# Kernel tuning notes

Measured on AMD Instinct MI355X. Metric: run time of the kernel, lower is better.

Reference implementation:

```python
import jax, jax.numpy as jnp
import numpy as np

B, N, CIN = 16, 2048, 6
R, G = 20, 128          # Reeb nodes, scc group size
F1 = 1000
NCLASS = 40


def pairwise_distance(pc):
    # pc: (B, N, C) -> adjacency exp(-squared_euclidean_dist), (B, N, N)
    inner = -2.0 * jnp.matmul(pc, pc.transpose(0, 2, 1))
    sq = jnp.sum(pc * pc, axis=-1, keepdims=True)
    return jnp.exp(-(sq + inner + sq.transpose(0, 2, 1)))


def get_laplacian(adj):
    # normalized Laplacian L = I - D^{-1/2} A D^{-1/2}
    d_inv = 1.0 / jnp.sqrt(jnp.sum(adj, axis=-1))
    eye = jnp.eye(adj.shape[-1], dtype=adj.dtype)
    return eye - d_inv[:, :, None] * adj * d_inv[:, None, :]


def cheb_conv(x, L, K, W, b):
    # Chebyshev recurrence: T0=x, T1=Lx, Tk=2L T_{k-1} - T_{k-2}
    xs = [x]
    if K > 1:
        x0, x1 = x, jnp.matmul(L, x)
        xs.append(x1)
        for _ in range(2, K):
            x2 = 2.0 * jnp.matmul(L, x1) - x0
            xs.append(x2)
            x0, x1 = x1, x2
    Bb, Nn, Fin = x.shape
    # torch stacks on dim0 then permutes to (B,N,Fin,K) before reshape -> K is minor axis
    xk = jnp.stack(xs, axis=-1).reshape(Bb, Nn, Fin * K)
    return jnp.matmul(xk, W) + b


def setup_inputs() -> dict:
    key = jax.random.key(0)
    ks = jax.random.split(key, 10)

    def glorot(k, shape):
        lim = np.sqrt(6.0 / (shape[0] + shape[1])).astype(np.float32)
        return jax.random.uniform(k, shape, jnp.float32, -lim, lim)

    return {
        "x": jax.random.normal(ks[0], (B, N, CIN), jnp.float32),
        "laplacian_Reeb": jax.random.normal(ks[1], (B, R, R), jnp.float32),
        "sccs": jax.random.randint(ks[2], (B, R, G), 0, N),
        "W1": glorot(ks[3], (CIN * 3, F1)), "b1": jnp.zeros((F1,), jnp.float32),
        "W2": glorot(ks[4], (F1 * 3, F1)), "b2": jnp.zeros((F1,), jnp.float32),
        "Wr": glorot(ks[5], (F1 * 6, F1)), "br": jnp.zeros((F1,), jnp.float32),
        "Wfc1": glorot(ks[6], (2 * F1, 512)), "bfc1": jnp.zeros((512,), jnp.float32),
        "Wfc2": glorot(ks[7], (512, 128)), "bfc2": jnp.zeros((128,), jnp.float32),
        "Wfc3": glorot(ks[8], (128, NCLASS)), "bfc3": jnp.zeros((NCLASS,), jnp.float32),
        "k": 30, "batch_size": B, "num_points": N,
    }


def reference(x, laplacian_Reeb, sccs, W1, b1, W2, b2, Wr, br,
              Wfc1, bfc1, Wfc2, bfc2, Wfc3, bfc3, k, batch_size, num_points):
    regs = []
    # graph Laplacian from point features (torch.no_grad)
    L = jax.lax.stop_gradient(get_laplacian(pairwise_distance(x)))
    out = jax.nn.relu(cheb_conv(x, L, 3, W1, b1))
    regs.append(jnp.linalg.norm(jnp.matmul(jnp.matmul(out.transpose(0, 2, 1), L), x)))

    # Reeb pooling: per Reeb node, max over its scc vertex group (torch.no_grad)
    v = out[jnp.arange(out.shape[0])[:, None, None], sccs]  # (B, R, G, F1)
    vertices_Reeb = jax.lax.stop_gradient(jnp.max(v, axis=2))  # (B, R, F1)

    # second dynamic-graph Laplacian on features (torch.no_grad)
    L2 = jax.lax.stop_gradient(get_laplacian(pairwise_distance(out)))
    out2 = jax.nn.relu(cheb_conv(out, L2, 3, W2, b2))
    regs.append(jnp.linalg.norm(jnp.matmul(jnp.matmul(out2.transpose(0, 2, 1), L2), x)))

    out_Reeb = jax.nn.relu(cheb_conv(vertices_Reeb, laplacian_Reeb, 6, Wr, br))

    g = jnp.max(out2, axis=1)           # (B, F1) global max pool
    g_Reeb = jnp.max(out_Reeb, axis=1)  # (B, F1)
    feat = jnp.concatenate([g_Reeb, g], axis=1)  # (B, 2000)

    h = jax.nn.relu(jnp.matmul(feat, Wfc1) + bfc1)
    regs += [jnp.sum(Wfc1[:, 0] ** 2), bfc1[0] ** 2]  # norm(weight.data[0])**2
    h = jax.nn.relu(jnp.matmul(h, Wfc2) + bfc2)
    regs += [jnp.sum(Wfc2[:, 0] ** 2), bfc2[0] ** 2]
    out_final = jnp.matmul(h, Wfc3) + bfc3
    regs += [jnp.sum(Wfc3[:, 0] ** 2), bfc3[0] ** 2]

    return out_final, jnp.stack(regs)
```

## Files before the change

kernel.cpp:

```cpp
#include <hip/hip_runtime.h>
#include <stdint.h>

#define DI __device__ __forceinline__

typedef __bf16 bf16x8 __attribute__((ext_vector_type(8)));
typedef float f32x4 __attribute__((ext_vector_type(4)));
typedef unsigned short u16x4 __attribute__((ext_vector_type(4)));
typedef unsigned short u16x8 __attribute__((ext_vector_type(8)));

static constexpr int BB = 16;
static constexpr int NP = 2048;
static constexpr int FP = 1024;
static constexpr int K3 = 3072;
static constexpr int RR = 20;
static constexpr int GG = 128;
static constexpr int RK = 6144;
static constexpr int MRp = 384;
static constexpr int NJ = 32;
static constexpr int NI = 8;
static constexpr int NJ2 = 8;

DI float b2f(unsigned short u) {
    unsigned v = ((unsigned)u) << 16;
    return __builtin_bit_cast(float, v);
}
DI unsigned short f2b(float f) {
    unsigned u = __builtin_bit_cast(unsigned, f);
    unsigned r = (u + 0x7FFFu + ((u >> 16) & 1u)) >> 16;
    return (unsigned short)r;
}

DI void glds16(const unsigned short* g, unsigned short* l) {
    __builtin_amdgcn_global_load_lds(
        (const __attribute__((address_space(1))) void*)g,
        (__attribute__((address_space(3))) void*)l, 16, 0, 0);
}

#define SYNC_VM4() asm volatile("s_waitcnt vmcnt(4)\n\ts_barrier" ::: "memory")
#define SYNC_VM0() asm volatile("s_waitcnt vmcnt(0)\n\ts_barrier" ::: "memory")
#define SYNC_LGKM() asm volatile("s_waitcnt lgkmcnt(0)\n\ts_barrier" ::: "memory")

enum { EADJ = 0, ELAP1 = 1, ELAP2 = 2, EBRELU = 3 };

template <int EPI>
__global__ __launch_bounds__(256) void gemm_bt(
    const unsigned short* __restrict__ A, long sA, int lda,
    const unsigned short* __restrict__ Bt, long sB, int ldb,
    unsigned short* __restrict__ C, long sC, int ldc, int K,
    const float* __restrict__ sq,
    float* __restrict__ rowsum,
    const unsigned short* __restrict__ aux, long sAux, int ldaux,
    const float* __restrict__ bias, int biasN)
{
    __shared__ unsigned short smem[16384];
    const int tid = threadIdx.x;

    int gx = gridDim.x, gy = gridDim.y;
    int flat = blockIdx.x + gx * (blockIdx.y + gy * blockIdx.z);
    int tpb = gx * gy;
    int T = tpb * gridDim.z;
    int bz, ty, tx;
    if (((T & 7) == 0) && ((gx & 7) == 0)) {
        int per = T >> 3;
        int g = (flat & 7) * per + (flat >> 3);
        bz = g / tpb;
        int t = g - bz * tpb;
        int strip = gy << 3;
        int cg = t / strip;
        int r = t - cg * strip;
        ty = r >> 3;
        tx = (cg << 3) + (r & 7);
    } else {
        bz = blockIdx.z; ty = blockIdx.y; tx = blockIdx.x;
    }
    const int rowBase = ty * 128;
    const int colBase = tx * 128;
    const unsigned short* Ab = A + (long)bz * sA + (long)rowBase * lda;
    const unsigned short* Bb = Bt + (long)bz * sB + (long)colBase * ldb;

    const int lane = tid & 63;
    const int q = lane >> 4;
    const int l15 = lane & 15;
    const int wave = tid >> 6;
    const int wr = (wave >> 1) * 64;
    const int wc = (wave & 1) * 64;

    const int r0 = tid & 127, c0 = tid >> 7;
    const int c1 = c0 + 2;

    f32x4 acc[4][4];
#pragma unroll
    for (int i = 0; i < 4; i++)
#pragma unroll
        for (int j = 0; j < 4; j++) acc[i][j] = f32x4{0.f, 0.f, 0.f, 0.f};

    const int nIter = K >> 5;
    glds16(Ab + (long)r0 * lda + c0 * 8, smem + tid * 8);
    glds16(Ab + (long)r0 * lda + c1 * 8, smem + (tid + 256) * 8);
    glds16(Bb + (long)r0 * ldb + c0 * 8, smem + 4096 + tid * 8);
    glds16(Bb + (long)r0 * ldb + c1 * 8, smem + 4096 + (tid + 256) * 8);

    for (int it = 0; it < nIter; ++it) {
        unsigned short* cur = smem + ((it & 1) << 13);
        unsigned short* nxt = smem + (((it + 1) & 1) << 13);
        if (it + 1 < nIter) {
            const int kb = (it + 1) << 5;
            glds16(Ab + (long)r0 * lda + kb + c0 * 8, nxt + tid * 8);
            glds16(Ab + (long)r0 * lda + kb + c1 * 8, nxt + (tid + 256) * 8);
            glds16(Bb + (long)r0 * ldb + kb + c0 * 8, nxt + 4096 + tid * 8);
            glds16(Bb + (long)r0 * ldb + kb + c1 * 8, nxt + 4096 + (tid + 256) * 8);
            SYNC_VM4();
        } else {
            SYNC_VM0();
        }
        bf16x8 af[4], bfr[4];
#pragma unroll
        for (int mi = 0; mi < 4; mi++)
            af[mi] = *(const bf16x8*)(cur + (q * 128 + wr + mi * 16 + l15) * 8);
#pragma unroll
        for (int ni = 0; ni < 4; ni++)
            bfr[ni] = *(const bf16x8*)(cur + 4096 + (q * 128 + wc + ni * 16 + l15) * 8);
#pragma unroll
        for (int mi = 0; mi < 4; mi++)
#pragma unroll
            for (int ni = 0; ni < 4; ni++)
                acc[mi][ni] = __builtin_amdgcn_mfma_f32_16x16x32_bf16(
                    af[mi], bfr[ni], acc[mi][ni], 0, 0, 0);
        SYNC_LGKM();
    }

    const float* sqb = (EPI != EBRELU) ? (sq + (long)bz * NP) : nullptr;
#pragma unroll
    for (int mi = 0; mi < 4; mi++) {
#pragma unroll
        for (int rg = 0; rg < 4; rg++) {
            const int grow = rowBase + wr + mi * 16 + q * 4 + rg;
            float rsumv = 0.f;
            float di = 0.f;
            if (EPI == ELAP1 || EPI == ELAP2) di = sqb[grow];
#pragma unroll
            for (int ni = 0; ni < 4; ni++) {
                const int gcol = colBase + wc + ni * 16 + l15;
                float v = acc[mi][ni][rg];
                long cidx = (long)bz * sC + (long)grow * ldc + gcol;
                if (EPI == EADJ) {
                    float e = __expf(2.f * v - sqb[grow] - sqb[gcol]);
                    C[cidx] = f2b(e);
                    rsumv += e;
                } else if (EPI == ELAP1) {
                    float o = b2f(aux[(long)bz * sAux + (long)grow * ldaux + gcol]);
                    C[cidx] = f2b(o - di * v);
                } else if (EPI == ELAP2) {
                    long abase = (long)bz * sAux + (long)grow * ldaux + gcol;
                    float o0 = b2f(aux[abase]);
                    float o1 = b2f(aux[abase + 1024]);
                    C[cidx] = f2b(2.f * (o1 - di * v) - o0);
                } else {
                    float bv = (gcol < biasN) ? bias[gcol] : 0.f;
                    float o = v + bv;
                    C[cidx] = f2b(o > 0.f ? o : 0.f);
                }
            }
            if (EPI == EADJ) {
                rsumv += __shfl_xor(rsumv, 1);
                rsumv += __shfl_xor(rsumv, 2);
                rsumv += __shfl_xor(rsumv, 4);
                rsumv += __shfl_xor(rsumv, 8);
                if (l15 == 0) atomicAdd(&rowsum[(long)bz * NP + grow], rsumv);
            }
        }
    }
}

__global__ __launch_bounds__(256) void k_trs(
    const unsigned short* __restrict__ src, long sS, int ldS,
    const float* __restrict__ dv,
    unsigned short* __restrict__ dst, long sD, int ldD)
{
    __shared__ unsigned short t[64][72];
    const int b = blockIdx.z;
    const int c0 = blockIdx.x * 64, r0 = blockIdx.y * 64;
    const unsigned short* S = src + (long)b * sS;
    const float* dvb = dv + (long)b * NP;
    unsigned short* D = dst + (long)b * sD;
    const int tx = threadIdx.x & 7, ty = threadIdx.x >> 3;
#pragma unroll
    for (int p = 0; p < 2; p++) {
        int r = ty + p * 32;
        float s = dvb[r0 + r];
        u16x8 v = *(const u16x8*)(S + (long)(r0 + r) * ldS + c0 + tx * 8);
#pragma unroll
        for (int k = 0; k < 8; k++) t[tx * 8 + k][r] = f2b(s * b2f(v[k]));
    }
    __syncthreads();
#pragma unroll
    for (int p = 0; p < 2; p++) {
        int r = ty + p * 32;
        u16x8 v;
#pragma unroll
        for (int k = 0; k < 8; k++) v[k] = t[r][tx * 8 + k];
        *(u16x8*)(D + (long)(c0 + r) * ldD + r0 + tx * 8) = v;
    }
}

__global__ void k_trf32(const float* __restrict__ src, int R, int C,
                        float* __restrict__ dst)
{
    __shared__ float t[32][33];
    const int c0 = blockIdx.x * 32, r0 = blockIdx.y * 32;
#pragma unroll
    for (int p = 0; p < 4; p++) {
        int r = r0 + threadIdx.y + p * 8;
        int c = c0 + threadIdx.x;
        t[threadIdx.y + p * 8][threadIdx.x] =
            (r < R && c < C) ? src[(long)r * C + c] : 0.f;
    }
    __syncthreads();
#pragma unroll
    for (int p = 0; p < 4; p++) {
        int c = c0 + threadIdx.y + p * 8;
        int r = r0 + threadIdx.x;
        if (c < C && r < R) dst[(long)c * R + r] = t[threadIdx.x][threadIdx.y + p * 8];
    }
}

__global__ __launch_bounds__(256) void k_wperm(
    const float* __restrict__ W, unsigned short* __restrict__ dst, int KK, int dstld)
{
    __shared__ float tile[64][65];
    const int o0 = blockIdx.x * 64;
    const int kk0 = blockIdx.y * 64;
    const int s = kk0 >> 10;
    const int fbase = kk0 & 1023;
    const int ci = threadIdx.x & 63;
    const int ri = threadIdx.x >> 6;
#pragma unroll 4
    for (int p = 0; p < 16; p++) {
        int fi = fbase + ri + p * 4;
        int oi = o0 + ci;
        float v = 0.f;
        if (fi < 1000 && oi < 1000) v = W[((long)fi * KK + s) * 1000 + oi];
        tile[ri + p * 4][ci] = v;
    }
    __syncthreads();
#pragma unroll 4
    for (int p = 0; p < 16; p++) {
        int orow = ri + p * 4;
        dst[(long)(o0 + orow) * dstld + kk0 + ci] = f2b(tile[ci][orow]);
    }
}

__global__ void k_zinit(float* __restrict__ rs2, float* __restrict__ g,
                        float* __restrict__ racc, unsigned short* __restrict__ catrpad,
                        float* __restrict__ dv1, float* __restrict__ xacc1,
                        float* __restrict__ xacc2, float* __restrict__ yacc1,
                        float* __restrict__ yacc2, float* __restrict__ l2acc,
                        float* __restrict__ vr)
{
    long i = (long)blockIdx.x * 256 + threadIdx.x;
    if (i < (long)BB * NP) { rs2[i] = 0.f; dv1[i] = 0.f; }
    if (i < (long)BB * FP) g[i] = 0.f;
    if (i < 64) racc[i] = 0.f;
    if (i < (long)(MRp - 320) * RK) catrpad[i] = 0;
    if (i < (long)BB * 6 * NP) { xacc1[i] = 0.f; xacc2[i] = 0.f; l2acc[i] = 0.f; }
    if (i < (long)BB * 6 * FP) { yacc1[i] = 0.f; yacc2[i] = 0.f; }
    if (i < (long)BB * RR * FP) vr[i] = 0.f;
}

__global__ void k_xprep(const float* __restrict__ x, float* __restrict__ x6t,
                        float* __restrict__ sqx)
{
    const int b = blockIdx.y;
    const int j = blockIdx.x * 256 + threadIdx.x;
    float s = 0.f;
#pragma unroll
    for (int c = 0; c < 6; c++) {
        float v = x[((long)b * NP + j) * 6 + c];
        x6t[(long)b * 6 * NP + c * NP + j] = v;
        s += v * v;
    }
    sqx[(long)b * NP + j] = s;
}

template <int MODE>
__global__ __launch_bounds__(256) void k_lapj(
    const float* __restrict__ x6t, const float* __restrict__ sqx,
    const float* __restrict__ dv1, const float* __restrict__ srct,
    float* __restrict__ acc)
{
    const int b = blockIdx.z;
    const int row = blockIdx.x * 256 + threadIdx.x;
    const int j0 = blockIdx.y * (NP / NJ);
    const float* xt = x6t + (long)b * 6 * NP;
    const float* sq = sqx + (long)b * NP;
    float xi[6];
#pragma unroll
    for (int c = 0; c < 6; c++) xi[c] = xt[c * NP + row];
    const float sqi = sq[row];
    const float* dv = (MODE >= 1) ? (dv1 + (long)b * NP) : nullptr;
    const float* st = (MODE >= 1) ? (srct + (long)b * 6 * NP) : nullptr;
    float s0 = 0.f;
    float sc[6] = {0, 0, 0, 0, 0, 0};
    for (int j = j0; j < j0 + NP / NJ; j++) {
        float dot = 0.f;
#pragma unroll
        for (int c = 0; c < 6; c++) dot += xi[c] * xt[c * NP + j];
        float e = __expf(2.f * dot - sqi - sq[j]);
        if (MODE == 0) {
            s0 += e;
        } else {
            float wgt = e * dv[j];
#pragma unroll
            for (int c = 0; c < 6; c++) sc[c] += wgt * st[c * NP + j];
        }
    }
    if (MODE == 0) {
        atomicAdd(&acc[(long)b * NP + row], s0);
    } else {
#pragma unroll
        for (int c = 0; c < 6; c++)
            atomicAdd(&acc[(long)b * 6 * NP + c * NP + row], sc[c]);
    }
}

template <int MODE>
__global__ void k_lfin(const float* __restrict__ x6t, const float* __restrict__ dv1,
                       const float* __restrict__ xacc, const float* __restrict__ x1t6,
                       float* __restrict__ outv)
{
    const int b = blockIdx.y;
    const int row = blockIdx.x * 256 + threadIdx.x;
    const float di = dv1[(long)b * NP + row];
#pragma unroll
    for (int c = 0; c < 6; c++) {
        long idx = (long)b * 6 * NP + c * NP + row;
        float xi = x6t[idx];
        float sc = xacc[idx];
        if (MODE == 1) outv[idx] = xi - di * sc;
        else           outv[idx] = 2.f * (x1t6[idx] - di * sc) - xi;
    }
}

__global__ __launch_bounds__(256) void k_adjx(
    const unsigned short* __restrict__ adj, const float* __restrict__ dv,
    const float* __restrict__ x6t, float* __restrict__ l2acc)
{
    __shared__ float xs[6][256];
    __shared__ float dvs[256];
    __shared__ float lsum[64][4][6];
    const int b = blockIdx.z;
    const int j0 = blockIdx.y * (NP / NJ2);
    if (threadIdx.x < 256) dvs[threadIdx.x] = dv[(long)b * NP + j0 + threadIdx.x];
    for (int e = threadIdx.x; e < 6 * 256; e += 256) {
        int c = e >> 8, j = e & 255;
        xs[c][j] = x6t[(long)b * 6 * NP + c * NP + j0 + j];
    }
    __syncthreads();
    const int ty = threadIdx.x >> 2;
    const int tx = threadIdx.x & 3;
    const int grow = blockIdx.x * 64 + ty;
    const unsigned short* rowp = adj + (long)b * NP * NP + (long)grow * NP + j0;
    float sc[6] = {0, 0, 0, 0, 0, 0};
    for (int it = 0; it < 8; it++) {
        int col = it * 32 + tx * 8;
        u16x8 a8 = *(const u16x8*)(rowp + col);
#pragma unroll
        for (int k = 0; k < 8; k++) {
            float w = b2f(a8[k]) * dvs[col + k];
#pragma unroll
            for (int c = 0; c < 6; c++) sc[c] += w * xs[c][col + k];
        }
    }
#pragma unroll
    for (int c = 0; c < 6; c++) lsum[ty][tx][c] = sc[c];
    __syncthreads();
    for (int e = threadIdx.x; e < 64 * 6; e += 256) {
        int row = e / 6, c = e % 6;
        float t = lsum[row][0][c] + lsum[row][1][c] + lsum[row][2][c] + lsum[row][3][c];
        atomicAdd(&l2acc[(long)b * 6 * NP + (long)c * NP + blockIdx.x * 64 + row], t);
    }
}

__global__ __launch_bounds__(256) void k_cheb1(
    const float* __restrict__ x, const float* __restrict__ x1t6,
    const float* __restrict__ x2t6, const float* __restrict__ W1,
    const float* __restrict__ b1, unsigned short* __restrict__ cat)
{
    __shared__ float xk[128 * 18];
    const int b = blockIdx.z;
    const int n0 = blockIdx.x * 128;
    const int f0 = blockIdx.y * 256;
    for (int e = threadIdx.x; e < 128 * 18; e += 256) {
        int rown = e / 18, c18 = e % 18;
        int cc = c18 / 3, kk = c18 % 3;
        int n = n0 + rown;
        float v;
        if (kk == 0) v = x[((long)b * NP + n) * 6 + cc];
        else if (kk == 1) v = x1t6[(long)b * 6 * NP + cc * NP + n];
        else v = x2t6[(long)b * 6 * NP + cc * NP + n];
        xk[e] = v;
    }
    __syncthreads();
    for (int gi = threadIdx.x; gi < 128 * 64; gi += 256) {
        int rown = gi >> 6;
        int f4 = f0 + (gi & 63) * 4;
        float a0 = 0, a1 = 0, a2 = 0, a3 = 0;
        if (f4 < 1000) {
            a0 = b1[f4]; a1 = b1[f4 + 1]; a2 = b1[f4 + 2]; a3 = b1[f4 + 3];
#pragma unroll
            for (int cI = 0; cI < 18; cI++) {
                float xv = xk[rown * 18 + cI];
                f32x4 w = *(const f32x4*)(W1 + cI * 1000 + f4);
                a0 += xv * w[0]; a1 += xv * w[1]; a2 += xv * w[2]; a3 += xv * w[3];
            }
            a0 = a0 > 0 ? a0 : 0; a1 = a1 > 0 ? a1 : 0;
            a2 = a2 > 0 ? a2 : 0; a3 = a3 > 0 ? a3 : 0;
        }
        u16x4 o;
        o[0] = f2b(a0); o[1] = f2b(a1); o[2] = f2b(a2); o[3] = f2b(a3);
        *(u16x4*)(cat + (long)b * NP * K3 + (long)(n0 + rown) * K3 + f4) = o;
    }
}

__global__ void k_sqc(const unsigned short* __restrict__ cat, float* __restrict__ sqc)
{
    __shared__ float red[256];
    const int b = blockIdx.y;
    const int rloc = threadIdx.x >> 4;
    const int r = blockIdx.x * 16 + rloc;
    const int tx = threadIdx.x & 15;
    const unsigned short* p = cat + (long)b * NP * K3 + (long)r * K3;
    float s = 0.f;
    for (int it = 0; it < 8; it++) {
        int cc = it * 128 + tx * 8;
        u16x8 v = *(const u16x8*)(p + cc);
#pragma unroll
        for (int k = 0; k < 8; k++) { float f = b2f(v[k]); s += f * f; }
    }
    red[threadIdx.x] = s;
    __syncthreads();
    if (tx == 0) {
        float t = 0.f;
#pragma unroll
        for (int k = 0; k < 16; k++) t += red[rloc * 16 + k];
        sqc[(long)b * NP + r] = t;
    }
}

__global__ void k_rsqrt(float* __restrict__ p) {
    int i = blockIdx.x * 256 + threadIdx.x;
    p[i] = rsqrtf(p[i]);
}

__global__ void k_vr(const unsigned short* __restrict__ cat,
                     const int* __restrict__ sccs, float* __restrict__ vr)
{
    const int b = blockIdx.y, r = blockIdx.x;
    const int g0 = blockIdx.z * (GG / 4);
    const int f4 = threadIdx.x * 4;
    const int* sp = sccs + ((long)b * RR + r) * GG;
    float m0 = 0.f, m1 = 0.f, m2 = 0.f, m3 = 0.f;
    for (int g = g0; g < g0 + GG / 4; g++) {
        int idx = sp[g];
        u16x4 v = *(const u16x4*)(cat + ((long)b * NP + idx) * K3 + f4);
        m0 = fmaxf(m0, b2f(v[0])); m1 = fmaxf(m1, b2f(v[1]));
        m2 = fmaxf(m2, b2f(v[2])); m3 = fmaxf(m3, b2f(v[3]));
    }
    float* op = vr + ((long)b * RR + r) * FP + f4;
    atomicMax((int*)&op[0], __float_as_int(m0));
    atomicMax((int*)&op[1], __float_as_int(m1));
    atomicMax((int*)&op[2], __float_as_int(m2));
    atomicMax((int*)&op[3], __float_as_int(m3));
}

__global__ __launch_bounds__(256) void k_reeb(
    const float* __restrict__ vr, const float* __restrict__ lapR,
    unsigned short* __restrict__ catr)
{
    __shared__ float Lr[RR * RR];
    const int b = blockIdx.y;
    for (int e = threadIdx.x; e < RR * RR; e += 256) Lr[e] = lapR[(long)b * RR * RR + e];
    __syncthreads();
    const int f = blockIdx.x * 256 + threadIdx.x;
    float xa[RR], xb[RR], xc[RR];
#pragma unroll
    for (int r = 0; r < RR; r++) xa[r] = vr[((long)b * RR + r) * FP + f];
#pragma unroll
    for (int r = 0; r < RR; r++) catr[((long)b * RR + r) * RK + f] = f2b(xa[r]);
#pragma unroll
    for (int r = 0; r < RR; r++) {
        float s = 0.f;
#pragma unroll
        for (int qq = 0; qq < RR; qq++) s += Lr[r * RR + qq] * xa[qq];
        xb[r] = s;
    }
#pragma unroll
    for (int r = 0; r < RR; r++) catr[((long)b * RR + r) * RK + FP + f] = f2b(xb[r]);
    for (int st = 2; st < 6; st++) {
#pragma unroll
        for (int r = 0; r < RR; r++) {
            float s = 0.f;
#pragma unroll
            for (int qq = 0; qq < RR; qq++) s += Lr[r * RR + qq] * xb[qq];
            xc[r] = 2.f * s - xa[r];
        }
#pragma unroll
        for (int r = 0; r < RR; r++)
            catr[((long)b * RR + r) * RK + st * FP + f] = f2b(xc[r]);
#pragma unroll
        for (int r = 0; r < RR; r++) { xa[r] = xb[r]; xb[r] = xc[r]; }
    }
}

__global__ void k_gmax(const unsigned short* __restrict__ out2, float* __restrict__ g)
{
    const int b = blockIdx.z;
    const int f = blockIdx.x * 256 + threadIdx.x;
    const int n0 = blockIdx.y * 256;
    float m = 0.f;
    for (int n = n0; n < n0 + 256; n++)
        m = fmaxf(m, b2f(out2[((long)b * NP + n) * FP + f]));
    if (f < 1000) atomicMax((int*)&g[(long)b * FP + f], __float_as_int(m));
}

__global__ void k_grmax(const unsigned short* __restrict__ outr, float* __restrict__ gr)
{
    const int b = blockIdx.y;
    const int f = blockIdx.x * 256 + threadIdx.x;
    float m = -1e30f;
    for (int r = 0; r < RR; r++)
        m = fmaxf(m, b2f(outr[((long)b * RR + r) * FP + f]));
    gr[(long)b * FP + f] = (f < 1000) ? m : 0.f;
}

__global__ __launch_bounds__(256) void k_rnacc(
    const unsigned short* __restrict__ mat, long sM, int ldm,
    const float* __restrict__ vt6, float* __restrict__ yacc)
{
    const int b = blockIdx.z;
    const int f = blockIdx.x * 256 + threadIdx.x;
    const int i0 = blockIdx.y * (NP / NI);
    const unsigned short* mp = mat + (long)b * sM + f;
    const float* vp = vt6 + (long)b * 6 * NP;
    float a[6] = {0, 0, 0, 0, 0, 0};
    for (int i = i0; i < i0 + NP / NI; i++) {
        float o = b2f(mp[(long)i * ldm]);
#pragma unroll
        for (int c = 0; c < 6; c++) a[c] += o * vp[c * NP + i];
    }
#pragma unroll
    for (int c = 0; c < 6; c++)
        atomicAdd(&yacc[((long)b * 6 + c) * FP + f], a[c]);
}

__global__ void k_rnred(const float* __restrict__ yacc1,
                        const float* __restrict__ yacc2, float* __restrict__ racc)
{
    __shared__ float red[256];
    const float* y = (blockIdx.x == 0) ? yacc1 : yacc2;
    const long tot = (long)BB * 6 * FP;
    const long per = tot / 16;
    const long e0 = blockIdx.y * per;
    float s = 0.f;
    for (long e = e0 + threadIdx.x; e < e0 + per; e += 256) {
        float v = y[e];
        s += v * v;
    }
    red[threadIdx.x] = s;
    __syncthreads();
    for (int st = 128; st > 0; st >>= 1) {
        if (threadIdx.x < st) red[threadIdx.x] += red[threadIdx.x + st];
        __syncthreads();
    }
    if (threadIdx.x == 0) atomicAdd(&racc[blockIdx.x], red[0]);
}

__global__ __launch_bounds__(256) void k_fc1w(
    const float* __restrict__ gr, const float* __restrict__ g,
    const float* __restrict__ WT1, const float* __restrict__ bias,
    float* __restrict__ h1)
{
    const int b = blockIdx.y;
    const int lane = threadIdx.x & 63;
    const int o = blockIdx.x * 4 + (threadIdx.x >> 6);
    const float* wt = WT1 + (long)o * 2000;
    const float* grp = gr + (long)b * FP;
    const float* gp = g + (long)b * FP;
    float s = 0.f;
    for (int j0 = 0; j0 < 2000; j0 += 64) {
        int j = j0 + lane;
        if (j < 2000) {
            float fv = (j < 1000) ? grp[j] : gp[j - 1000];
            s += fv * wt[j];
        }
    }
#pragma unroll
    for (int d = 1; d < 64; d <<= 1) s += __shfl_xor(s, d);
    if (lane == 0) {
        float v = s + bias[o];
        h1[(long)b * 512 + o] = v > 0.f ? v : 0.f;
    }
}

__global__ __launch_bounds__(256) void k_fc2w(
    const float* __restrict__ h1, const float* __restrict__ WT2,
    const float* __restrict__ bias, float* __restrict__ h2)
{
    const int b = blockIdx.y;
    const int lane = threadIdx.x & 63;
    const int o = blockIdx.x * 4 + (threadIdx.x >> 6);
    const float* wt = WT2 + (long)o * 512;
    const float* hp = h1 + (long)b * 512;
    float s = 0.f;
#pragma unroll
    for (int j0 = 0; j0 < 512; j0 += 64) s += hp[j0 + lane] * wt[j0 + lane];
#pragma unroll
    for (int d = 1; d < 64; d <<= 1) s += __shfl_xor(s, d);
    if (lane == 0) {
        float v = s + bias[o];
        h2[(long)b * 128 + o] = v > 0.f ? v : 0.f;
    }
}

__global__ void k_tail(const float* __restrict__ h2, const float* __restrict__ Wfc3,
                       const float* __restrict__ bfc3, const float* __restrict__ Wfc1,
                       const float* __restrict__ bfc1, const float* __restrict__ Wfc2,
                       const float* __restrict__ bfc2, const float* __restrict__ racc,
                       float* __restrict__ out)
{
    if (blockIdx.x == 0) {
        for (int e = threadIdx.x; e < 640; e += 256) {
            int row = e / 40, o = e % 40;
            float s = bfc3[o];
            for (int j = 0; j < 128; j++) s += h2[row * 128 + j] * Wfc3[j * 40 + o];
            out[e] = s;
        }
        return;
    }
    __shared__ float red[256];
    float s = 0.f;
    if (blockIdx.x == 1) {
        for (int j = threadIdx.x; j < 2000; j += 256) { float w = Wfc1[j * 512]; s += w * w; }
    } else if (blockIdx.x == 2) {
        for (int j = threadIdx.x; j < 512; j += 256) { float w = Wfc2[j * 128]; s += w * w; }
    } else {
        for (int j = threadIdx.x; j < 128; j += 256) { float w = Wfc3[j * 40]; s += w * w; }
    }
    red[threadIdx.x] = s;
    __syncthreads();
    for (int st = 128; st > 0; st >>= 1) {
        if (threadIdx.x < st) red[threadIdx.x] += red[threadIdx.x + st];
        __syncthreads();
    }
    if (threadIdx.x == 0) {
        if (blockIdx.x == 1) out[642] = red[0];
        else if (blockIdx.x == 2) out[644] = red[0];
        else {
            out[646] = red[0];
            out[640] = sqrtf(racc[0]);
            out[641] = sqrtf(racc[1]);
            out[643] = bfc1[0] * bfc1[0];
            out[645] = bfc2[0] * bfc2[0];
            out[647] = bfc3[0] * bfc3[0];
        }
    }
}

extern "C" void kernel_launch(void* const* d_in, const int* in_sizes, int n_in,
                              void* d_out, int out_size, void* d_ws, size_t ws_size,
                              hipStream_t stream)
{
    (void)in_sizes; (void)n_in; (void)out_size;
    const float* x    = (const float*)d_in[0];
    const float* lapR = (const float*)d_in[1];
    const int*   sccs = (const int*)d_in[2];
    const float* W1   = (const float*)d_in[3];
    const float* b1   = (const float*)d_in[4];
    const float* W2   = (const float*)d_in[5];
    const float* b2   = (const float*)d_in[6];
    const float* Wr   = (const float*)d_in[7];
    const float* br   = (const float*)d_in[8];
    const float* Wfc1 = (const float*)d_in[9];
    const float* bfc1 = (const float*)d_in[10];
    const float* Wfc2 = (const float*)d_in[11];
    const float* bfc2 = (const float*)d_in[12];
    const float* Wfc3 = (const float*)d_in[13];
    const float* bfc3 = (const float*)d_in[14];
    float* out = (float*)d_out;

    char* w = (char*)d_ws;
    size_t used = 0;
    auto alloc = [&](size_t bytes) {
        char* p = w + used;
        used += (bytes + 255) & ~(size_t)255;
        return p;
    };
    unsigned short* w2pt = (unsigned short*)alloc((size_t)FP * K3 * 2);
    unsigned short* wrpt = (unsigned short*)alloc((size_t)FP * RK * 2);
    unsigned short* catr = (unsigned short*)alloc((size_t)MRp * RK * 2);
    unsigned short* outr = (unsigned short*)alloc((size_t)MRp * FP * 2);
    float* vr   = (float*)alloc((size_t)BB * RR * FP * 4);
    float* x6t  = (float*)alloc((size_t)BB * 6 * NP * 4);
    float* sqx  = (float*)alloc((size_t)BB * NP * 4);
    float* dv1  = (float*)alloc((size_t)BB * NP * 4);
    float* x1t6 = (float*)alloc((size_t)BB * 6 * NP * 4);
    float* x2t6 = (float*)alloc((size_t)BB * 6 * NP * 4);
    float* xacc1= (float*)alloc((size_t)BB * 6 * NP * 4);
    float* xacc2= (float*)alloc((size_t)BB * 6 * NP * 4);
    float* l2acc= (float*)alloc((size_t)BB * 6 * NP * 4);
    float* sqc  = (float*)alloc((size_t)BB * NP * 4);
    float* rs2  = (float*)alloc((size_t)BB * NP * 4);
    float* l2xt6= (float*)alloc((size_t)BB * 6 * NP * 4);
    float* g    = (float*)alloc((size_t)BB * FP * 4);
    float* gr   = (float*)alloc((size_t)BB * FP * 4);
    float* h1   = (float*)alloc((size_t)BB * 512 * 4);
    float* h2   = (float*)alloc((size_t)BB * 128 * 4);
    float* racc = (float*)alloc(256);
    float* WT1  = (float*)alloc((size_t)512 * 2000 * 4);
    float* WT2  = (float*)alloc((size_t)128 * 512 * 4);
    float* yacc1= (float*)alloc((size_t)BB * 6 * FP * 4);
    float* yacc2= (float*)alloc((size_t)BB * 6 * FP * 4);

    const size_t PCAT = (size_t)NP * K3 * 2;
    const size_t PA   = (size_t)NP * NP * 2;
    const size_t PTT  = (size_t)FP * NP * 2;
    int C = 16;
    while (C > 1 && used + (size_t)C * (PCAT + PA + PTT) + 4096 > ws_size) C >>= 1;
    if (used + (size_t)C * (PCAT + PA + PTT) + 4096 > ws_size) return;

    unsigned short* cat_c = (unsigned short*)alloc((size_t)C * PCAT);
    unsigned short* a_c   = (unsigned short*)alloc((size_t)C * PA);
    unsigned short* tt_c  = (unsigned short*)alloc((size_t)C * PTT);
    unsigned short* out2_c = a_c;

    const long sCat = (long)NP * K3;
    const long sL2  = (long)NP * NP;
    const long sTT  = (long)FP * NP;
    const long sO2  = (long)NP * FP;

    k_zinit<<<dim3(1536), 256, 0, stream>>>(rs2, g, racc, catr + (size_t)320 * RK,
                                            dv1, xacc1, xacc2, yacc1, yacc2, l2acc, vr);

    k_wperm<<<dim3(16, K3 / 64), 256, 0, stream>>>(W2, w2pt, 3, K3);
    k_wperm<<<dim3(16, RK / 64), 256, 0, stream>>>(Wr, wrpt, 6, RK);
    k_trf32<<<dim3(16, 63), dim3(32, 8), 0, stream>>>(Wfc1, 2000, 512, WT1);
    k_trf32<<<dim3(4, 16), dim3(32, 8), 0, stream>>>(Wfc2, 512, 128, WT2);

    k_xprep<<<dim3(8, BB), 256, 0, stream>>>(x, x6t, sqx);
    k_lapj<0><<<dim3(8, NJ, BB), 256, 0, stream>>>(x6t, sqx, nullptr, nullptr, dv1);
    k_rsqrt<<<dim3(BB * NP / 256), 256, 0, stream>>>(dv1);
    k_lapj<1><<<dim3(8, NJ, BB), 256, 0, stream>>>(x6t, sqx, dv1, x6t, xacc1);
    k_lfin<1><<<dim3(8, BB), 256, 0, stream>>>(x6t, dv1, xacc1, nullptr, x1t6);
    k_lapj<2><<<dim3(8, NJ, BB), 256, 0, stream>>>(x6t, sqx, dv1, x1t6, xacc2);
    k_lfin<2><<<dim3(8, BB), 256, 0, stream>>>(x6t, dv1, xacc2, x1t6, x2t6);

    for (int c0 = 0; c0 < BB; c0 += C) {
        const float* xc  = x     + (long)c0 * NP * 6;
        const float* x6c = x6t   + (long)c0 * 6 * NP;
        const float* x1c = x1t6  + (long)c0 * 6 * NP;
        const float* x2c = x2t6  + (long)c0 * 6 * NP;
        float*       sqcc= sqc   + (long)c0 * NP;
        float*       rsc = rs2   + (long)c0 * NP;
        float*       l2ac= l2acc + (long)c0 * 6 * NP;
        float*       l2xc= l2xt6 + (long)c0 * 6 * NP;

        k_cheb1<<<dim3(16, 4, C), 256, 0, stream>>>(xc, x1c, x2c, W1, b1, cat_c);
        k_sqc<<<dim3(NP / 16, C), 256, 0, stream>>>(cat_c, sqcc);

        gemm_bt<EADJ><<<dim3(16, 16, C), 256, 0, stream>>>(
            cat_c, sCat, K3, cat_c, sCat, K3, a_c, sL2, NP, FP,
            sqcc, rsc, nullptr, 0, 0, nullptr, 0);
        k_rsqrt<<<dim3(C * NP / 256), 256, 0, stream>>>(rsc);

        k_adjx<<<dim3(NP / 64, NJ2, C), 256, 0, stream>>>(a_c, rsc, x6c, l2ac);
        k_lfin<1><<<dim3(8, C), 256, 0, stream>>>(x6c, rsc, l2ac, nullptr, l2xc);

        k_trs<<<dim3(16, 32, C), 256, 0, stream>>>(cat_c, sCat, K3, rsc, tt_c, sTT, NP);
        gemm_bt<ELAP1><<<dim3(8, 16, C), 256, 0, stream>>>(
            a_c, sL2, NP, tt_c, sTT, NP, cat_c + 1024, sCat, K3, NP,
            rsc, nullptr, cat_c, sCat, K3, nullptr, 0);

        k_trs<<<dim3(16, 32, C), 256, 0, stream>>>(cat_c + 1024, sCat, K3, rsc, tt_c, sTT, NP);
        gemm_bt<ELAP2><<<dim3(8, 16, C), 256, 0, stream>>>(
            a_c, sL2, NP, tt_c, sTT, NP, cat_c + 2048, sCat, K3, NP,
            rsc, nullptr, cat_c, sCat, K3, nullptr, 0);

        gemm_bt<EBRELU><<<dim3(8, 16, C), 256, 0, stream>>>(
            cat_c, sCat, K3, w2pt, 0, K3, out2_c, sO2, FP, K3,
            nullptr, nullptr, nullptr, 0, 0, b2, 1000);

        k_vr<<<dim3(RR, C, 4), 256, 0, stream>>>(
            cat_c, sccs + (long)c0 * RR * GG, vr + (long)c0 * RR * FP);
        k_gmax<<<dim3(4, 8, C), 256, 0, stream>>>(out2_c, g + (long)c0 * FP);
        k_rnacc<<<dim3(4, NI, C), 256, 0, stream>>>(
            cat_c, sCat, K3, x1c, yacc1 + (long)c0 * 6 * FP);
        k_rnacc<<<dim3(4, NI, C), 256, 0, stream>>>(
            out2_c, sO2, FP, l2xc, yacc2 + (long)c0 * 6 * FP);
    }

    k_reeb<<<dim3(4, BB), 256, 0, stream>>>(vr, lapR, catr);
    gemm_bt<EBRELU><<<dim3(8, 3, 1), 256, 0, stream>>>(
        catr, 0, RK, wrpt, 0, RK, outr, 0, FP, RK,
        nullptr, nullptr, nullptr, 0, 0, br, 1000);
    k_grmax<<<dim3(4, BB), 256, 0, stream>>>(outr, gr);

    k_rnred<<<dim3(2, 16), 256, 0, stream>>>(yacc1, yacc2, racc);
    k_fc1w<<<dim3(128, BB), 256, 0, stream>>>(gr, g, WT1, bfc1, h1);
    k_fc2w<<<dim3(32, BB), 256, 0, stream>>>(h1, WT2, bfc2, h2);
    k_tail<<<dim3(4), 256, 0, stream>>>(h2, Wfc3, bfc3, Wfc1, bfc1, Wfc2, bfc2, racc, out);
}
```

Before: 2.235 ms.

## Exploit adjacency symmetry, fuse row norms and global max, split-K Reeb GEMM

The adjacency GEMM now computes only the upper-triangular 128x128 tiles (136 of 256). Each off-diagonal tile is also written transposed through padded shared memory, and its column sums are added into the row sums. The squared-norm kernel is folded into the Chebyshev layer-1 kernel, and the global max over out2 is folded into the regularizer accumulation kernel. The small Reeb GEMM is split four ways along K with fp32 atomics, followed by a bias/ReLU finish kernel. These changes remove redundant GEMM work and extra passes over memory, at the cost of atomics, a larger shared buffer and a serial tile-index decode.

```diff
diff --git a/kernel.cpp b/kernel.cpp
--- a/kernel.cpp
+++ b/kernel.cpp
@@ -19,6 +19,7 @@
 static constexpr int NJ = 32;
 static constexpr int NI = 8;
 static constexpr int NJ2 = 8;
+static constexpr int TPAD = 132;
 
 DI float b2f(unsigned short u) {
     unsigned v = ((unsigned)u) << 16;
@@ -40,7 +41,7 @@
 #define SYNC_VM0() asm volatile("s_waitcnt vmcnt(0)\n\ts_barrier" ::: "memory")
 #define SYNC_LGKM() asm volatile("s_waitcnt lgkmcnt(0)\n\ts_barrier" ::: "memory")
 
-enum { EADJ = 0, ELAP1 = 1, ELAP2 = 2, EBRELU = 3 };
+enum { EADJ = 0, ELAP1 = 1, ELAP2 = 2, EBRELU = 3, EACCR = 4 };
 
 template <int EPI>
 __global__ __launch_bounds__(256) void gemm_bt(
@@ -52,7 +53,7 @@
     const unsigned short* __restrict__ aux, long sAux, int ldaux,
     const float* __restrict__ bias, int biasN)
 {
-    __shared__ unsigned short smem[16384];
+    __shared__ unsigned short smem[128 * TPAD];
     const int tid = threadIdx.x;
 
     int gx = gridDim.x, gy = gridDim.y;
@@ -73,10 +74,26 @@
     } else {
         bz = blockIdx.z; ty = blockIdx.y; tx = blockIdx.x;
     }
+    bool diag = true;
+    if (EPI == EADJ) {
+        int t = tx;
+        int qx = 0;
+        while ((qx + 1) * (qx + 2) / 2 <= t) qx++;
+        ty = t - qx * (qx + 1) / 2;
+        tx = qx;
+        diag = (ty == tx);
+    }
     const int rowBase = ty * 128;
     const int colBase = tx * 128;
-    const unsigned short* Ab = A + (long)bz * sA + (long)rowBase * lda;
-    const unsigned short* Bb = Bt + (long)bz * sB + (long)colBase * ldb;
+    const unsigned short* Ab;
+    const unsigned short* Bb;
+    if (EPI == EACCR) {
+        Ab = A + (long)rowBase * lda + (long)bz * K;
+        Bb = Bt + (long)colBase * ldb + (long)bz * K;
+    } else {
+        Ab = A + (long)bz * sA + (long)rowBase * lda;
+        Bb = Bt + (long)bz * sB + (long)colBase * ldb;
+    }
 
     const int lane = tid & 63;
     const int q = lane >> 4;
@@ -129,7 +146,10 @@
         SYNC_LGKM();
     }
 
-    const float* sqb = (EPI != EBRELU) ? (sq + (long)bz * NP) : nullptr;
+    if (EPI == EADJ) __syncthreads();
+
+    const float* sqb = (EPI == EADJ || EPI == ELAP1 || EPI == ELAP2)
+                           ? (sq + (long)bz * NP) : nullptr;
 #pragma unroll
     for (int mi = 0; mi < 4; mi++) {
 #pragma unroll
@@ -145,8 +165,14 @@
                 long cidx = (long)bz * sC + (long)grow * ldc + gcol;
                 if (EPI == EADJ) {
                     float e = __expf(2.f * v - sqb[grow] - sqb[gcol]);
-                    C[cidx] = f2b(e);
+                    unsigned short h = f2b(e);
+                    C[cidx] = h;
                     rsumv += e;
+                    if (!diag) {
+                        const int rl = wr + mi * 16 + q * 4 + rg;
+                        const int cl = wc + ni * 16 + l15;
+                        smem[cl * TPAD + rl] = h;
+                    }
                 } else if (EPI == ELAP1) {
                     float o = b2f(aux[(long)bz * sAux + (long)grow * ldaux + gcol]);
                     C[cidx] = f2b(o - di * v);
@@ -155,10 +181,12 @@
                     float o0 = b2f(aux[abase]);
                     float o1 = b2f(aux[abase + 1024]);
                     C[cidx] = f2b(2.f * (o1 - di * v) - o0);
-                } else {
+                } else if (EPI == EBRELU) {
                     float bv = (gcol < biasN) ? bias[gcol] : 0.f;
                     float o = v + bv;
                     C[cidx] = f2b(o > 0.f ? o : 0.f);
+                } else {
+                    atomicAdd(&rowsum[(long)grow * ldc + gcol], v);
                 }
             }
             if (EPI == EADJ) {
@@ -168,6 +196,29 @@
                 rsumv += __shfl_xor(rsumv, 8);
                 if (l15 == 0) atomicAdd(&rowsum[(long)bz * NP + grow], rsumv);
             }
+        }
+    }
+
+    if (EPI == EADJ) {
+        if (!diag) {
+            __syncthreads();
+            const int cl = tid >> 1, hh = tid & 1;
+            const unsigned short* srcp = smem + cl * TPAD + hh * 64;
+            unsigned short* dstp = C + (long)bz * sC + (long)(colBase + cl) * ldc
+                                 + rowBase + hh * 64;
+            float csum = 0.f;
+#pragma unroll
+            for (int k2 = 0; k2 < 8; k2++) {
+                u16x4 v0 = *(const u16x4*)(srcp + k2 * 8);
+                u16x4 v1 = *(const u16x4*)(srcp + k2 * 8 + 4);
+                u16x8 vv;
+                vv[0] = v0[0]; vv[1] = v0[1]; vv[2] = v0[2]; vv[3] = v0[3];
+                vv[4] = v1[0]; vv[5] = v1[1]; vv[6] = v1[2]; vv[7] = v1[3];
+#pragma unroll
+                for (int e2 = 0; e2 < 8; e2++) csum += b2f(vv[e2]);
+                *(u16x8*)(dstp + k2 * 8) = vv;
+            }
+            atomicAdd(&rowsum[(long)bz * NP + colBase + cl], csum);
         }
     }
 }
@@ -255,16 +306,18 @@
                         float* __restrict__ dv1, float* __restrict__ xacc1,
                         float* __restrict__ xacc2, float* __restrict__ yacc1,
                         float* __restrict__ yacc2, float* __restrict__ l2acc,
-                        float* __restrict__ vr)
+                        float* __restrict__ vr, float* __restrict__ sqc,
+                        float* __restrict__ accR)
 {
     long i = (long)blockIdx.x * 256 + threadIdx.x;
-    if (i < (long)BB * NP) { rs2[i] = 0.f; dv1[i] = 0.f; }
+    if (i < (long)BB * NP) { rs2[i] = 0.f; dv1[i] = 0.f; sqc[i] = 0.f; }
     if (i < (long)BB * FP) g[i] = 0.f;
     if (i < 64) racc[i] = 0.f;
     if (i < (long)(MRp - 320) * RK) catrpad[i] = 0;
     if (i < (long)BB * 6 * NP) { xacc1[i] = 0.f; xacc2[i] = 0.f; l2acc[i] = 0.f; }
     if (i < (long)BB * 6 * FP) { yacc1[i] = 0.f; yacc2[i] = 0.f; }
     if (i < (long)BB * RR * FP) vr[i] = 0.f;
+    if (i < (long)MRp * FP) accR[i] = 0.f;
 }
 
 __global__ void k_xprep(const float* __restrict__ x, float* __restrict__ x6t,
@@ -384,9 +437,11 @@
 __global__ __launch_bounds__(256) void k_cheb1(
     const float* __restrict__ x, const float* __restrict__ x1t6,
     const float* __restrict__ x2t6, const float* __restrict__ W1,
-    const float* __restrict__ b1, unsigned short* __restrict__ cat)
+    const float* __restrict__ b1, unsigned short* __restrict__ cat,
+    float* __restrict__ sqc)
 {
     __shared__ float xk[128 * 18];
+    __shared__ float rs[128];
     const int b = blockIdx.z;
     const int n0 = blockIdx.x * 128;
     const int f0 = blockIdx.y * 256;
@@ -400,7 +455,9 @@
         else v = x2t6[(long)b * 6 * NP + cc * NP + n];
         xk[e] = v;
     }
-    __syncthreads();
+    if (threadIdx.x < 128) rs[threadIdx.x] = 0.f;
+    __syncthreads();
+    const int lane = threadIdx.x & 63;
     for (int gi = threadIdx.x; gi < 128 * 64; gi += 256) {
         int rown = gi >> 6;
         int f4 = f0 + (gi & 63) * 4;
@@ -419,32 +476,15 @@
         u16x4 o;
         o[0] = f2b(a0); o[1] = f2b(a1); o[2] = f2b(a2); o[3] = f2b(a3);
         *(u16x4*)(cat + (long)b * NP * K3 + (long)(n0 + rown) * K3 + f4) = o;
-    }
-}
-
-__global__ void k_sqc(const unsigned short* __restrict__ cat, float* __restrict__ sqc)
-{
-    __shared__ float red[256];
-    const int b = blockIdx.y;
-    const int rloc = threadIdx.x >> 4;
-    const int r = blockIdx.x * 16 + rloc;
-    const int tx = threadIdx.x & 15;
-    const unsigned short* p = cat + (long)b * NP * K3 + (long)r * K3;
-    float s = 0.f;
-    for (int it = 0; it < 8; it++) {
-        int cc = it * 128 + tx * 8;
-        u16x8 v = *(const u16x8*)(p + cc);
-#pragma unroll
-        for (int k = 0; k < 8; k++) { float f = b2f(v[k]); s += f * f; }
-    }
-    red[threadIdx.x] = s;
-    __syncthreads();
-    if (tx == 0) {
-        float t = 0.f;
-#pragma unroll
-        for (int k = 0; k < 16; k++) t += red[rloc * 16 + k];
-        sqc[(long)b * NP + r] = t;
-    }
+        float r0 = b2f(o[0]), r1 = b2f(o[1]), r2 = b2f(o[2]), r3 = b2f(o[3]);
+        float s2 = r0 * r0 + r1 * r1 + r2 * r2 + r3 * r3;
+#pragma unroll
+        for (int d = 1; d < 64; d <<= 1) s2 += __shfl_xor(s2, d);
+        if (lane == 0) atomicAdd(&rs[rown], s2);
+    }
+    __syncthreads();
+    if (threadIdx.x < 128)
+        atomicAdd(&sqc[(long)b * NP + n0 + threadIdx.x], rs[threadIdx.x]);
 }
 
 __global__ void k_rsqrt(float* __restrict__ p) {
@@ -512,15 +552,14 @@
     }
 }
 
-__global__ void k_gmax(const unsigned short* __restrict__ out2, float* __restrict__ g)
-{
-    const int b = blockIdx.z;
+__global__ void k_rfin(const float* __restrict__ accR, const float* __restrict__ br,
+                       unsigned short* __restrict__ outr)
+{
     const int f = blockIdx.x * 256 + threadIdx.x;
-    const int n0 = blockIdx.y * 256;
-    float m = 0.f;
-    for (int n = n0; n < n0 + 256; n++)
-        m = fmaxf(m, b2f(out2[((long)b * NP + n) * FP + f]));
-    if (f < 1000) atomicMax((int*)&g[(long)b * FP + f], __float_as_int(m));
+    const int m = blockIdx.y;
+    float bv = (f < 1000) ? br[f] : 0.f;
+    float v = accR[(long)m * FP + f] + bv;
+    outr[(long)m * FP + f] = f2b(v > 0.f ? v : 0.f);
 }
 
 __global__ void k_grmax(const unsigned short* __restrict__ outr, float* __restrict__ gr)
@@ -535,7 +574,8 @@
 
 __global__ __launch_bounds__(256) void k_rnacc(
     const unsigned short* __restrict__ mat, long sM, int ldm,
-    const float* __restrict__ vt6, float* __restrict__ yacc)
+    const float* __restrict__ vt6, float* __restrict__ yacc,
+    float* __restrict__ gm)
 {
     const int b = blockIdx.z;
     const int f = blockIdx.x * 256 + threadIdx.x;
@@ -543,14 +583,17 @@
     const unsigned short* mp = mat + (long)b * sM + f;
     const float* vp = vt6 + (long)b * 6 * NP;
     float a[6] = {0, 0, 0, 0, 0, 0};
+    float mx = 0.f;
     for (int i = i0; i < i0 + NP / NI; i++) {
         float o = b2f(mp[(long)i * ldm]);
+        if (gm) mx = fmaxf(mx, o);
 #pragma unroll
         for (int c = 0; c < 6; c++) a[c] += o * vp[c * NP + i];
     }
 #pragma unroll
     for (int c = 0; c < 6; c++)
         atomicAdd(&yacc[((long)b * 6 + c) * FP + f], a[c]);
+    if (gm) atomicMax((int*)&gm[(long)b * FP + f], __float_as_int(mx));
 }
 
 __global__ void k_rnred(const float* __restrict__ yacc1,
@@ -699,6 +742,7 @@
     unsigned short* wrpt = (unsigned short*)alloc((size_t)FP * RK * 2);
     unsigned short* catr = (unsigned short*)alloc((size_t)MRp * RK * 2);
     unsigned short* outr = (unsigned short*)alloc((size_t)MRp * FP * 2);
+    float* accR = (float*)alloc((size_t)MRp * FP * 4);
     float* vr   = (float*)alloc((size_t)BB * RR * FP * 4);
     float* x6t  = (float*)alloc((size_t)BB * 6 * NP * 4);
     float* sqx  = (float*)alloc((size_t)BB * NP * 4);
@@ -739,7 +783,8 @@
     const long sO2  = (long)NP * FP;
 
     k_zinit<<<dim3(1536), 256, 0, stream>>>(rs2, g, racc, catr + (size_t)320 * RK,
-                                            dv1, xacc1, xacc2, yacc1, yacc2, l2acc, vr);
+                                            dv1, xacc1, xacc2, yacc1, yacc2, l2acc,
+                                            vr, sqc, accR);
 
     k_wperm<<<dim3(16, K3 / 64), 256, 0, stream>>>(W2, w2pt, 3, K3);
     k_wperm<<<dim3(16, RK / 64), 256, 0, stream>>>(Wr, wrpt, 6, RK);
@@ -764,10 +809,9 @@
         float*       l2ac= l2acc + (long)c0 * 6 * NP;
         float*       l2xc= l2xt6 + (long)c0 * 6 * NP;
 
-        k_cheb1<<<dim3(16, 4, C), 256, 0, stream>>>(xc, x1c, x2c, W1, b1, cat_c);
-        k_sqc<<<dim3(NP / 16, C), 256, 0, stream>>>(cat_c, sqcc);
-
-        gemm_bt<EADJ><<<dim3(16, 16, C), 256, 0, stream>>>(
+        k_cheb1<<<dim3(16, 4, C), 256, 0, stream>>>(xc, x1c, x2c, W1, b1, cat_c, sqcc);
+
+        gemm_bt<EADJ><<<dim3(136, 1, C), 256, 0, stream>>>(
             cat_c, sCat, K3, cat_c, sCat, K3, a_c, sL2, NP, FP,
             sqcc, rsc, nullptr, 0, 0, nullptr, 0);
         k_rsqrt<<<dim3(C * NP / 256), 256, 0, stream>>>(rsc);
@@ -791,17 +835,17 @@
 
         k_vr<<<dim3(RR, C, 4), 256, 0, stream>>>(
             cat_c, sccs + (long)c0 * RR * GG, vr + (long)c0 * RR * FP);
-        k_gmax<<<dim3(4, 8, C), 256, 0, stream>>>(out2_c, g + (long)c0 * FP);
         k_rnacc<<<dim3(4, NI, C), 256, 0, stream>>>(
-            cat_c, sCat, K3, x1c, yacc1 + (long)c0 * 6 * FP);
+            cat_c, sCat, K3, x1c, yacc1 + (long)c0 * 6 * FP, nullptr);
         k_rnacc<<<dim3(4, NI, C), 256, 0, stream>>>(
-            out2_c, sO2, FP, l2xc, yacc2 + (long)c0 * 6 * FP);
+            out2_c, sO2, FP, l2xc, yacc2 + (long)c0 * 6 * FP, g + (long)c0 * FP);
     }
 
     k_reeb<<<dim3(4, BB), 256, 0, stream>>>(vr, lapR, catr);
-    gemm_bt<EBRELU><<<dim3(8, 3, 1), 256, 0, stream>>>(
-        catr, 0, RK, wrpt, 0, RK, outr, 0, FP, RK,
-        nullptr, nullptr, nullptr, 0, 0, br, 1000);
+    gemm_bt<EACCR><<<dim3(8, 3, 4), 256, 0, stream>>>(
+        catr, 0, RK, wrpt, 0, RK, outr, 0, FP, RK / 4,
+        nullptr, accR, nullptr, 0, 0, nullptr, 0);
+    k_rfin<<<dim3(4, 320), 256, 0, stream>>>(accR, br, outr);
     k_grmax<<<dim3(4, BB), 256, 0, stream>>>(outr, gr);
 
     k_rnred<<<dim3(2, 16), 256, 0, stream>>>(yacc1, yacc2, racc);
```

Result: faster. 1.955 ms (-12.5%).
